# Kernel optimization log

Hardware: AMD Instinct MI355X
Metric: run time of the kernel (lower is better)

## Reference

```python
import jax, jax.numpy as jnp
import numpy as np

MODEL_DIM = 1024
NUM_HEADS = 16
HEAD_DIM = MODEL_DIM // NUM_HEADS
B, SQ, SK = 1, 4096, 4096


def setup_inputs() -> dict:
    key = jax.random.key(0)
    ks = jax.random.split(key, 10)
    s = 0.02  # realistic init scale for weights
    inp = {
        "x_query": jax.random.normal(ks[0], (B, SQ, MODEL_DIM), jnp.float32),
        "x_context": jax.random.normal(ks[1], (B, SK, MODEL_DIM), jnp.float32),
        # causal mask [B,1,Sq,Sk]; 0 -> masked
        "mask": jnp.tril(jnp.ones((SQ, SK), jnp.int32))[None, None, :, :],
        "wq": jax.random.normal(ks[2], (MODEL_DIM, MODEL_DIM), jnp.float32) * s,
        "bq": jnp.zeros((MODEL_DIM,), jnp.float32),
        "wk": jax.random.normal(ks[3], (MODEL_DIM, MODEL_DIM), jnp.float32) * s,
        "bk": jnp.zeros((MODEL_DIM,), jnp.float32),
        "wv": jax.random.normal(ks[4], (MODEL_DIM, MODEL_DIM), jnp.float32) * s,
        "bv": jnp.zeros((MODEL_DIM,), jnp.float32),
        "wo": jax.random.normal(ks[5], (MODEL_DIM, MODEL_DIM), jnp.float32) * s,
        "bo": jnp.zeros((MODEL_DIM,), jnp.float32),
    }
    return inp


def reference(x_query, x_context, mask, wq, bq, wk, bk, wv, bv, wo, bo):
    b = x_query.shape[0]
    # torch nn.Linear: y = x @ W.T + b
    q = x_query @ wq.T + bq
    k = x_context @ wk.T + bk
    v = x_context @ wv.T + bv
    # [B, S, D] -> [B, H, S, Hd]
    def split_heads(t):
        return t.reshape(b, -1, NUM_HEADS, HEAD_DIM).transpose(0, 2, 1, 3)
    q, k, v = split_heads(q), split_heads(k), split_heads(v)
    scale = 1.0 / jnp.sqrt(jnp.asarray(HEAD_DIM, q.dtype))
    scores = jnp.einsum('bhqd,bhkd->bhqk', q, k) * scale  # [B,H,Sq,Sk]
    scores = jnp.where(mask == 0, jnp.asarray(-1e9, scores.dtype), scores)
    attn = jax.nn.softmax(scores, axis=-1)
    # dropout: eval mode (identity)
    ctx = jnp.einsum('bhqk,bhkd->bhqd', attn, v)
    ctx = ctx.transpose(0, 2, 1, 3).reshape(b, -1, MODEL_DIM)
    return ctx @ wo.T + bo
```

## Files before the change

kernel.cpp:

```cpp
#include <hip/hip_runtime.h>

typedef __bf16 bf16x8 __attribute__((ext_vector_type(8)));
typedef float f32x4 __attribute__((ext_vector_type(4)));
typedef float f32x16 __attribute__((ext_vector_type(16)));
typedef unsigned int u32x2v __attribute__((ext_vector_type(2)));

#define GLD16(gp, lp) __builtin_amdgcn_global_load_lds( \
    (const __attribute__((address_space(1))) void*)(gp), \
    (__attribute__((address_space(3))) void*)(lp), 16, 0, 0)

__device__ __forceinline__ unsigned short f2bf(float f) {
  unsigned int u = __float_as_uint(f);
  u += 0x7FFFu + ((u >> 16) & 1u);
  return (unsigned short)(u >> 16);
}

__device__ __forceinline__ unsigned int cvtpk(float lo, float hi) {
  unsigned int r;
  asm("v_cvt_pk_bf16_f32 %0, %1, %2" : "=v"(r) : "v"(lo), "v"(hi));
  return r;
}

__device__ __forceinline__ float exp2f_(float x) {
#if __has_builtin(__builtin_amdgcn_exp2f)
  return __builtin_amdgcn_exp2f(x);
#else
  float r; asm("v_exp_f32 %0, %1" : "=v"(r) : "v"(x)); return r;
#endif
}

__device__ __forceinline__ u32x2v pswap(unsigned int a, unsigned int b) {
#if __has_builtin(__builtin_amdgcn_permlane32_swap)
  u32x2v r;
  auto q = __builtin_amdgcn_permlane32_swap(a, b, false, false);
  r[0] = q[0]; r[1] = q[1];
  return r;
#else
  unsigned int pa = (unsigned int)__shfl_xor((int)a, 32);
  unsigned int pb = (unsigned int)__shfl_xor((int)b, 32);
  int hi = (threadIdx.x >> 5) & 1;
  u32x2v r;
  r[0] = hi ? pb : a;
  r[1] = hi ? b : pa;
  return r;
#endif
}

__global__ __launch_bounds__(256) void cast6(
    const float* __restrict__ xq, const float* __restrict__ xc,
    const float* __restrict__ wq, const float* __restrict__ wk,
    const float* __restrict__ wv, const float* __restrict__ wo,
    unsigned short* __restrict__ d) {
  int i = (blockIdx.x * 256 + threadIdx.x) * 4;
  const float* s; int off;
  if      (i < (4 << 20))  { s = xq; off = 0; }
  else if (i < (8 << 20))  { s = xc; off = 4 << 20; }
  else if (i < (9 << 20))  { s = wq; off = 8 << 20; }
  else if (i < (10 << 20)) { s = wk; off = 9 << 20; }
  else if (i < (11 << 20)) { s = wv; off = 10 << 20; }
  else                     { s = wo; off = 11 << 20; }
  float4 v = *(const float4*)(s + (i - off));
  ushort4 o;
  o.x = f2bf(v.x); o.y = f2bf(v.y); o.z = f2bf(v.z); o.w = f2bf(v.w);
  *(ushort4*)(d + i) = o;
}

template<int OUTF32>
__device__ __forceinline__ void gemm_body(
    const unsigned short* __restrict__ A, const unsigned short* __restrict__ B,
    const float* __restrict__ bias, void* __restrict__ C,
    int N, int K, int bm, int bn, float scale,
    unsigned short* As, unsigned short* Bs) {
  const int t = threadIdx.x;
  const int lane = t & 63, wid = t >> 6;
  const int wm = wid >> 1, wn = wid & 1;
  const int l15 = lane & 15, l4 = lane >> 4, l7 = lane & 7;

  f32x4 acc[4][4];
#pragma unroll
  for (int i = 0; i < 4; ++i)
#pragma unroll
    for (int j = 0; j < 4; ++j) acc[i][j] = (f32x4){0.f, 0.f, 0.f, 0.f};

  const char* Ab = (const char*)A;
  const char* Bb = (const char*)B;
  const int ldb = K * 2;

  for (int kt = 0; kt < K; kt += 64) {
#pragma unroll
    for (int c = 0; c < 4; ++c) {
      int o = c * 4096 + wid * 1024 + lane * 16;
      int row = o >> 7;
      int ch = ((o >> 4) & 7) ^ (row & 7);
      const char* ga = Ab + (size_t)(bm * 128 + row) * ldb + kt * 2 + ch * 16;
      GLD16(ga, (char*)As + c * 4096 + wid * 1024);
      const char* gb = Bb + (size_t)(bn * 128 + row) * ldb + kt * 2 + ch * 16;
      GLD16(gb, (char*)Bs + c * 4096 + wid * 1024);
    }
    __syncthreads();
#pragma unroll
    for (int kk = 0; kk < 2; ++kk) {
      bf16x8 af[4], bfr[4];
#pragma unroll
      for (int mi = 0; mi < 4; ++mi) {
        int row = wm * 64 + mi * 16 + l15;
        int ch = (l4 + 4 * kk) ^ l7;
        af[mi] = *(const bf16x8*)((const char*)As + row * 128 + ch * 16);
      }
#pragma unroll
      for (int ni = 0; ni < 4; ++ni) {
        int row = wn * 64 + ni * 16 + l15;
        int ch = (l4 + 4 * kk) ^ l7;
        bfr[ni] = *(const bf16x8*)((const char*)Bs + row * 128 + ch * 16);
      }
#pragma unroll
      for (int mi = 0; mi < 4; ++mi)
#pragma unroll
        for (int ni = 0; ni < 4; ++ni)
          acc[mi][ni] = __builtin_amdgcn_mfma_f32_16x16x32_bf16(
              af[mi], bfr[ni], acc[mi][ni], 0, 0, 0);
    }
    __syncthreads();
  }

#pragma unroll
  for (int ni = 0; ni < 4; ++ni) {
    int col = bn * 128 + wn * 64 + ni * 16 + l15;
    float bv = bias[col];
#pragma unroll
    for (int mi = 0; mi < 4; ++mi) {
#pragma unroll
      for (int r = 0; r < 4; ++r) {
        int row = bm * 128 + wm * 64 + mi * 16 + l4 * 4 + r;
        float v = (acc[mi][ni][r] + bv) * scale;
        if (OUTF32) ((float*)C)[(size_t)row * N + col] = v;
        else ((unsigned short*)C)[(size_t)row * N + col] = f2bf(v);
      }
    }
  }
}

__global__ __launch_bounds__(256) void gemm_qkv(
    const unsigned short* __restrict__ xq, const unsigned short* __restrict__ xc,
    const unsigned short* __restrict__ wq, const unsigned short* __restrict__ wk,
    const unsigned short* __restrict__ wv,
    const float* __restrict__ bq, const float* __restrict__ bk,
    const float* __restrict__ bv,
    unsigned short* __restrict__ Qo, unsigned short* __restrict__ Ko,
    unsigned short* __restrict__ Vo) {
  __shared__ __align__(16) unsigned short As[128 * 64];
  __shared__ __align__(16) unsigned short Bs[128 * 64];
  const unsigned short* A; const unsigned short* B; const float* bias;
  unsigned short* C; float scale;
  if (blockIdx.z == 0)      { A = xq; B = wq; bias = bq; C = Qo; scale = 0.18033688011112042f; }
  else if (blockIdx.z == 1) { A = xc; B = wk; bias = bk; C = Ko; scale = 1.0f; }
  else                      { A = xc; B = wv; bias = bv; C = Vo; scale = 1.0f; }
  gemm_body<0>(A, B, bias, (void*)C, 1024, 1024, blockIdx.y, blockIdx.x, scale, As, Bs);
}

__global__ __launch_bounds__(256) void gemm_out(
    const unsigned short* __restrict__ A, const unsigned short* __restrict__ B,
    const float* __restrict__ bias, float* __restrict__ C) {
  __shared__ __align__(16) unsigned short As[128 * 64];
  __shared__ __align__(16) unsigned short Bs[128 * 64];
  gemm_body<1>(A, B, bias, (void*)C, 1024, 1024, blockIdx.y, blockIdx.x, 1.0f, As, Bs);
}

__global__ __launch_bounds__(512)
__attribute__((amdgpu_waves_per_eu(4, 4)))
void flash_attn(
    const unsigned short* __restrict__ Q, const unsigned short* __restrict__ K,
    const unsigned short* __restrict__ V, unsigned short* __restrict__ O) {
  __shared__ __align__(16) char smem[65536];

  const int wgid = blockIdx.x;
  int h, qb;
  if (wgid < 256) { h = wgid & 15; qb = wgid >> 4; }
  else            { int r = wgid - 256; h = r & 15; qb = 31 - (r >> 4); }

  const int t = threadIdx.x;
  const int lane = t & 63, w = t >> 6;
  const int hf = w >> 2;
  const int s = w & 3;
  const int tl = t & 255;
  const int l31 = lane & 31, hi = lane >> 5;
  const int q0w = qb * 128 + s * 32;
  const int qwmax = q0w + 31;
  const int nh = qb + 1;
  const int tbase = hf ? nh : 0;

  bf16x8 qf[4];
#pragma unroll
  for (int ks = 0; ks < 4; ++ks)
    qf[ks] = *(const bf16x8*)(Q + (size_t)(q0w + l31) * 1024 + h * 64 + ks * 16 + hi * 8);

  f32x16 po0, po1;
#pragma unroll
  for (int r = 0; r < 16; ++r) { po0[r] = 0.f; po1[r] = 0.f; }
  float m_i = -1e30f, l_i = 0.f;

  const int vd4 = (tl & 15) * 4;
  const int vkvr = (tl >> 4) * 4;
  uint2 va[4];

  auto stageK = [&](int tile, int buf) {
#pragma unroll
    for (int i = 0; i < 2; ++i) {
      int id = i * 256 + tl;
      int row = id >> 3;
      int ch = (id & 7) ^ (row & 7);
      GLD16((const char*)K + (size_t)(tile * 64 + row) * 2048 + h * 128 + ch * 16,
            smem + (hf * 2 + buf) * 8192 + id * 16);
    }
  };
  auto loadV = [&](int tile) {
#pragma unroll
    for (int i = 0; i < 4; ++i)
      va[i] = *(const uint2*)(V + (size_t)(tile * 64 + vkvr + i) * 1024 + h * 64 + vd4);
  };
  auto writeV = [&](int buf) {
    char* Vt = smem + 32768 + (hf * 2 + buf) * 8192;
#pragma unroll
    for (int j = 0; j < 4; ++j) {
      unsigned sel = (j & 1) ? 0x07060302u : 0x05040100u;
      unsigned s01 = (j < 2) ? __builtin_amdgcn_perm(va[1].x, va[0].x, sel)
                             : __builtin_amdgcn_perm(va[1].y, va[0].y, sel);
      unsigned s23 = (j < 2) ? __builtin_amdgcn_perm(va[3].x, va[2].x, sel)
                             : __builtin_amdgcn_perm(va[3].y, va[2].y, sel);
      int row = vd4 + j;
      int sw = (vkvr * 2) ^ (((row >> 2) & 7) << 4);
      *(uint2*)(Vt + row * 128 + sw) = make_uint2(s01, s23);
    }
  };

  stageK(tbase, 0);
  loadV(tbase);
  writeV(0);
  __syncthreads();

  for (int it = 0; it < nh; ++it) {
    const int c = it & 1;
    const bool pf = (it + 1) < nh;
    if (pf) { stageK(tbase + it + 1, c ^ 1); loadV(tbase + it + 1); }

    const int kv0 = (tbase + it) * 64;
    if (kv0 <= qwmax) {
      const char* Ks = smem + (hf * 2 + c) * 8192;
      const char* Vt = smem + 32768 + (hf * 2 + c) * 8192;
      f32x16 s0, s1;
#pragma unroll
      for (int r = 0; r < 16; ++r) { s0[r] = 0.f; s1[r] = 0.f; }
      __builtin_amdgcn_s_setprio(1);
#pragma unroll
      for (int ks = 0; ks < 4; ++ks) {
        int c0 = ((ks * 2 + hi) ^ (l31 & 7)) << 4;
        bf16x8 k0 = *(const bf16x8*)(Ks + l31 * 128 + c0);
        bf16x8 k1 = *(const bf16x8*)(Ks + (32 + l31) * 128 + c0);
        s0 = __builtin_amdgcn_mfma_f32_32x32x16_bf16(k0, qf[ks], s0, 0, 0, 0);
        s1 = __builtin_amdgcn_mfma_f32_32x32x16_bf16(k1, qf[ks], s1, 0, 0, 0);
      }
      __builtin_amdgcn_s_setprio(0);
      if (kv0 + 63 > q0w) {
        int q = q0w + l31;
#pragma unroll
        for (int r = 0; r < 16; ++r) {
          int kvi = kv0 + (r & 3) + 8 * (r >> 2) + 4 * hi;
          if (kvi > q) s0[r] = -1e30f;
          if (kvi + 32 > q) s1[r] = -1e30f;
        }
      }
      float mx[16];
#pragma unroll
      for (int i = 0; i < 8; ++i) {
        mx[i] = fmaxf(s0[2 * i], s0[2 * i + 1]);
        mx[8 + i] = fmaxf(s1[2 * i], s1[2 * i + 1]);
      }
#pragma unroll
      for (int i = 0; i < 8; ++i) mx[i] = fmaxf(mx[i], mx[8 + i]);
#pragma unroll
      for (int i = 0; i < 4; ++i) mx[i] = fmaxf(mx[i], mx[4 + i]);
      float mt = fmaxf(fmaxf(mx[0], mx[1]), fmaxf(mx[2], mx[3]));
      u32x2v mw = pswap(__float_as_uint(mt), __float_as_uint(mt));
      mt = fmaxf(__uint_as_float(mw[0]), __uint_as_float(mw[1]));
      if (!__all(mt - m_i <= 8.0f)) {
        float mn = fmaxf(m_i, mt);
        float corr = exp2f_(m_i - mn);
        m_i = mn;
        l_i *= corr;
#pragma unroll
        for (int r = 0; r < 16; ++r) { po0[r] *= corr; po1[r] *= corr; }
      }
#pragma unroll
      for (int r = 0; r < 16; ++r) s0[r] = exp2f_(s0[r] - m_i);
#pragma unroll
      for (int r = 0; r < 16; ++r) s1[r] = exp2f_(s1[r] - m_i);
      float sx[16];
#pragma unroll
      for (int i = 0; i < 8; ++i) {
        sx[i] = s0[2 * i] + s0[2 * i + 1];
        sx[8 + i] = s1[2 * i] + s1[2 * i + 1];
      }
#pragma unroll
      for (int i = 0; i < 8; ++i) sx[i] += sx[8 + i];
#pragma unroll
      for (int i = 0; i < 4; ++i) sx[i] += sx[4 + i];
      float ps = (sx[0] + sx[1]) + (sx[2] + sx[3]);
      u32x2v sw2 = pswap(__float_as_uint(ps), __float_as_uint(ps));
      l_i += __uint_as_float(sw2[0]) + __uint_as_float(sw2[1]);

#pragma unroll
      for (int kp = 0; kp < 4; ++kp) {
        const f32x16& sv = (kp < 2) ? s0 : s1;
        const int b = (kp & 1) * 8;
        unsigned c0v = cvtpk(sv[b + 0], sv[b + 1]);
        unsigned c1v = cvtpk(sv[b + 2], sv[b + 3]);
        unsigned c2v = cvtpk(sv[b + 4], sv[b + 5]);
        unsigned c3v = cvtpk(sv[b + 6], sv[b + 7]);
        u32x2v w02 = pswap(c0v, c2v);
        u32x2v w13 = pswap(c1v, c3v);
        union { unsigned u[4]; bf16x8 v; } pfr;
        pfr.u[0] = w02[0]; pfr.u[1] = w13[0]; pfr.u[2] = w02[1]; pfr.u[3] = w13[1];
        int cb = kp * 2 + hi;
        __builtin_amdgcn_s_setprio(1);
        {
          int row = l31;
          bf16x8 vf = *(const bf16x8*)(Vt + row * 128 + ((cb ^ ((row >> 2) & 7)) << 4));
          po0 = __builtin_amdgcn_mfma_f32_32x32x16_bf16(vf, pfr.v, po0, 0, 0, 0);
        }
        {
          int row = 32 + l31;
          bf16x8 vf = *(const bf16x8*)(Vt + row * 128 + ((cb ^ ((row >> 2) & 7)) << 4));
          po1 = __builtin_amdgcn_mfma_f32_32x32x16_bf16(vf, pfr.v, po1, 0, 0, 0);
        }
        __builtin_amdgcn_s_setprio(0);
      }
    }
    if (pf) writeV(c ^ 1);
    __syncthreads();
  }

  char* mrg = smem + 16384;
  if (hf) {
    char* mb = mrg + s * 9216 + lane * 144;
    *(f32x16*)(mb) = po0;
    *(f32x16*)(mb + 64) = po1;
    *(float*)(mb + 128) = m_i;
    *(float*)(mb + 132) = l_i;
  }
  __syncthreads();
  float rinv = 0.f;
  if (!hf) {
    char* mb = mrg + s * 9216 + lane * 144;
    float pm = *(float*)(mb + 128);
    float plv = *(float*)(mb + 132);
    float M = fmaxf(m_i, pm);
    float wA = exp2f_(m_i - M);
    float wB = exp2f_(pm - M);
    float lt = l_i * wA + plv * wB;
    rinv = 1.0f / lt;
    f32x16 qa = *(const f32x16*)(mb);
#pragma unroll
    for (int r = 0; r < 16; ++r) po0[r] = po0[r] * wA + qa[r] * wB;
    f32x16 qbv = *(const f32x16*)(mb + 64);
#pragma unroll
    for (int r = 0; r < 16; ++r) po1[r] = po1[r] * wA + qbv[r] * wB;

    int qlocal = s * 32 + l31;
#pragma unroll
    for (int g = 0; g < 4; ++g) {
#pragma unroll
      for (int db = 0; db < 2; ++db) {
        const f32x16& p = db ? po1 : po0;
        unsigned w0 = cvtpk(p[g * 4 + 0] * rinv, p[g * 4 + 1] * rinv);
        unsigned w1 = cvtpk(p[g * 4 + 2] * rinv, p[g * 4 + 3] * rinv);
        int d0 = db * 32 + 8 * g + 4 * hi;
        int byte = qlocal * 128 + ((d0 * 2) ^ ((qlocal & 7) << 4));
        *(uint2*)(smem + byte) = make_uint2(w0, w1);
      }
    }
  }
  __syncthreads();
  if (!hf) {
#pragma unroll
    for (int it = 0; it < 4; ++it) {
      int r = it * 32 + (t >> 3);
      int c = t & 7;
      uint4 val = *(const uint4*)(smem + r * 128 + ((c ^ (r & 7)) << 4));
      *(uint4*)((char*)O + (size_t)(qb * 128 + r) * 2048 + h * 128 + c * 16) = val;
    }
  }
}

extern "C" void kernel_launch(void* const* d_in, const int* in_sizes, int n_in,
                              void* d_out, int out_size, void* d_ws, size_t ws_size,
                              hipStream_t stream) {
  const float* xq = (const float*)d_in[0];
  const float* xc = (const float*)d_in[1];
  const float* wq = (const float*)d_in[3];
  const float* bq = (const float*)d_in[4];
  const float* wk = (const float*)d_in[5];
  const float* bk = (const float*)d_in[6];
  const float* wv = (const float*)d_in[7];
  const float* bv = (const float*)d_in[8];
  const float* wo = (const float*)d_in[9];
  const float* bo = (const float*)d_in[10];

  unsigned short* wsb = (unsigned short*)d_ws;
  unsigned short* xqb = wsb;
  unsigned short* xcb = wsb + (4 << 20);
  unsigned short* wqb = wsb + (8 << 20);
  unsigned short* wkb = wsb + (9 << 20);
  unsigned short* wvb = wsb + (10 << 20);
  unsigned short* wob = wsb + (11 << 20);
  unsigned short* Qb  = wsb + (12 << 20);
  unsigned short* Kb  = wsb + (16 << 20);
  unsigned short* Vb  = wsb + (20 << 20);
  unsigned short* Cb  = wsb + (24 << 20);

  cast6<<<12288, 256, 0, stream>>>(xq, xc, wq, wk, wv, wo, wsb);

  dim3 gq(1024 / 128, 4096 / 128, 3);
  gemm_qkv<<<gq, 256, 0, stream>>>(xqb, xcb, wqb, wkb, wvb, bq, bk, bv, Qb, Kb, Vb);

  flash_attn<<<512, 512, 0, stream>>>(Qb, Kb, Vb, Cb);

  dim3 go(1024 / 128, 4096 / 128);
  gemm_out<<<go, 256, 0, stream>>>(Cb, wob, bo, (float*)d_out);
}
```

Measured before the change: 160.7 us.

## Split long causal attention rows across two workgroups with atomic-flag merge

Changes the flash-attention work split. Instead of pairing a short and a long query block in one workgroup, short query blocks run alone and the long ones (qb >= 17) are split across two workgroups, which merge partial outputs through global scratch plus an atomic counter; the last one to arrive combines and stores. This aims to balance per-workgroup work and fill more CUs with 752 workgroups. The cost is an extra memset, fp32 partial writes and reads through global memory, and a scratch area that reuses the workspace where the bf16 casts of the inputs live (already consumed by that point).

```diff
diff --git a/kernel.cpp b/kernel.cpp
--- a/kernel.cpp
+++ b/kernel.cpp
@@ -166,17 +166,20 @@
   gemm_body<1>(A, B, bias, (void*)C, 1024, 1024, blockIdx.y, blockIdx.x, 1.0f, As, Bs);
 }
 
-__global__ __launch_bounds__(512)
-__attribute__((amdgpu_waves_per_eu(4, 4)))
+__global__ __launch_bounds__(512, 4)
 void flash_attn(
     const unsigned short* __restrict__ Q, const unsigned short* __restrict__ K,
-    const unsigned short* __restrict__ V, unsigned short* __restrict__ O) {
+    const unsigned short* __restrict__ V, unsigned short* __restrict__ O,
+    float* __restrict__ partO, float* __restrict__ mlBase,
+    int* __restrict__ flags) {
   __shared__ __align__(16) char smem[65536];
 
-  const int wgid = blockIdx.x;
-  int h, qb;
-  if (wgid < 256) { h = wgid & 15; qb = wgid >> 4; }
-  else            { int r = wgid - 256; h = r & 15; qb = 31 - (r >> 4); }
+  const int b = blockIdx.x;
+  const int h = b & 15;
+  const int e = 46 - (b >> 4);
+  int qb, role, nsplit;
+  if (e < 17) { qb = e; role = 0; nsplit = 1; }
+  else        { qb = 17 + ((e - 17) >> 1); role = (e - 17) & 1; nsplit = 2; }
 
   const int t = threadIdx.x;
   const int lane = t & 63, w = t >> 6;
@@ -186,8 +189,12 @@
   const int l31 = lane & 31, hi = lane >> 5;
   const int q0w = qb * 128 + s * 32;
   const int qwmax = q0w + 31;
-  const int nh = qb + 1;
-  const int tbase = hf ? nh : 0;
+
+  const int t0 = (nsplit == 2) ? role * (qb + 1) : 0;
+  const int n  = (nsplit == 2) ? (qb + 1) : 2 * (qb + 1);
+  const int nA = (n + 1) >> 1;
+  const int my_n = hf ? (n - nA) : nA;
+  const int my_t0 = t0 + (hf ? nA : 0);
 
   bf16x8 qf[4];
 #pragma unroll
@@ -233,109 +240,109 @@
     }
   };
 
-  stageK(tbase, 0);
-  loadV(tbase);
-  writeV(0);
+  if (my_n > 0) { stageK(my_t0, 0); loadV(my_t0); writeV(0); }
   __syncthreads();
 
-  for (int it = 0; it < nh; ++it) {
+  for (int it = 0; it < nA; ++it) {
     const int c = it & 1;
-    const bool pf = (it + 1) < nh;
-    if (pf) { stageK(tbase + it + 1, c ^ 1); loadV(tbase + it + 1); }
-
-    const int kv0 = (tbase + it) * 64;
-    if (kv0 <= qwmax) {
-      const char* Ks = smem + (hf * 2 + c) * 8192;
-      const char* Vt = smem + 32768 + (hf * 2 + c) * 8192;
-      f32x16 s0, s1;
-#pragma unroll
-      for (int r = 0; r < 16; ++r) { s0[r] = 0.f; s1[r] = 0.f; }
-      __builtin_amdgcn_s_setprio(1);
-#pragma unroll
-      for (int ks = 0; ks < 4; ++ks) {
-        int c0 = ((ks * 2 + hi) ^ (l31 & 7)) << 4;
-        bf16x8 k0 = *(const bf16x8*)(Ks + l31 * 128 + c0);
-        bf16x8 k1 = *(const bf16x8*)(Ks + (32 + l31) * 128 + c0);
-        s0 = __builtin_amdgcn_mfma_f32_32x32x16_bf16(k0, qf[ks], s0, 0, 0, 0);
-        s1 = __builtin_amdgcn_mfma_f32_32x32x16_bf16(k1, qf[ks], s1, 0, 0, 0);
-      }
-      __builtin_amdgcn_s_setprio(0);
-      if (kv0 + 63 > q0w) {
-        int q = q0w + l31;
-#pragma unroll
-        for (int r = 0; r < 16; ++r) {
-          int kvi = kv0 + (r & 3) + 8 * (r >> 2) + 4 * hi;
-          if (kvi > q) s0[r] = -1e30f;
-          if (kvi + 32 > q) s1[r] = -1e30f;
-        }
-      }
-      float mx[16];
-#pragma unroll
-      for (int i = 0; i < 8; ++i) {
-        mx[i] = fmaxf(s0[2 * i], s0[2 * i + 1]);
-        mx[8 + i] = fmaxf(s1[2 * i], s1[2 * i + 1]);
-      }
-#pragma unroll
-      for (int i = 0; i < 8; ++i) mx[i] = fmaxf(mx[i], mx[8 + i]);
-#pragma unroll
-      for (int i = 0; i < 4; ++i) mx[i] = fmaxf(mx[i], mx[4 + i]);
-      float mt = fmaxf(fmaxf(mx[0], mx[1]), fmaxf(mx[2], mx[3]));
-      u32x2v mw = pswap(__float_as_uint(mt), __float_as_uint(mt));
-      mt = fmaxf(__uint_as_float(mw[0]), __uint_as_float(mw[1]));
-      if (!__all(mt - m_i <= 8.0f)) {
-        float mn = fmaxf(m_i, mt);
-        float corr = exp2f_(m_i - mn);
-        m_i = mn;
-        l_i *= corr;
-#pragma unroll
-        for (int r = 0; r < 16; ++r) { po0[r] *= corr; po1[r] *= corr; }
-      }
-#pragma unroll
-      for (int r = 0; r < 16; ++r) s0[r] = exp2f_(s0[r] - m_i);
-#pragma unroll
-      for (int r = 0; r < 16; ++r) s1[r] = exp2f_(s1[r] - m_i);
-      float sx[16];
-#pragma unroll
-      for (int i = 0; i < 8; ++i) {
-        sx[i] = s0[2 * i] + s0[2 * i + 1];
-        sx[8 + i] = s1[2 * i] + s1[2 * i + 1];
-      }
-#pragma unroll
-      for (int i = 0; i < 8; ++i) sx[i] += sx[8 + i];
-#pragma unroll
-      for (int i = 0; i < 4; ++i) sx[i] += sx[4 + i];
-      float ps = (sx[0] + sx[1]) + (sx[2] + sx[3]);
-      u32x2v sw2 = pswap(__float_as_uint(ps), __float_as_uint(ps));
-      l_i += __uint_as_float(sw2[0]) + __uint_as_float(sw2[1]);
-
-#pragma unroll
-      for (int kp = 0; kp < 4; ++kp) {
-        const f32x16& sv = (kp < 2) ? s0 : s1;
-        const int b = (kp & 1) * 8;
-        unsigned c0v = cvtpk(sv[b + 0], sv[b + 1]);
-        unsigned c1v = cvtpk(sv[b + 2], sv[b + 3]);
-        unsigned c2v = cvtpk(sv[b + 4], sv[b + 5]);
-        unsigned c3v = cvtpk(sv[b + 6], sv[b + 7]);
-        u32x2v w02 = pswap(c0v, c2v);
-        u32x2v w13 = pswap(c1v, c3v);
-        union { unsigned u[4]; bf16x8 v; } pfr;
-        pfr.u[0] = w02[0]; pfr.u[1] = w13[0]; pfr.u[2] = w02[1]; pfr.u[3] = w13[1];
-        int cb = kp * 2 + hi;
+    const bool pfv = (it + 1) < my_n;
+    if (pfv) { stageK(my_t0 + it + 1, c ^ 1); loadV(my_t0 + it + 1); }
+
+    if (it < my_n) {
+      const int kv0 = (my_t0 + it) * 64;
+      if (kv0 <= qwmax) {
+        const char* Ks = smem + (hf * 2 + c) * 8192;
+        const char* Vt = smem + 32768 + (hf * 2 + c) * 8192;
+        f32x16 s0, s1;
+#pragma unroll
+        for (int r = 0; r < 16; ++r) { s0[r] = 0.f; s1[r] = 0.f; }
         __builtin_amdgcn_s_setprio(1);
-        {
-          int row = l31;
-          bf16x8 vf = *(const bf16x8*)(Vt + row * 128 + ((cb ^ ((row >> 2) & 7)) << 4));
-          po0 = __builtin_amdgcn_mfma_f32_32x32x16_bf16(vf, pfr.v, po0, 0, 0, 0);
-        }
-        {
-          int row = 32 + l31;
-          bf16x8 vf = *(const bf16x8*)(Vt + row * 128 + ((cb ^ ((row >> 2) & 7)) << 4));
-          po1 = __builtin_amdgcn_mfma_f32_32x32x16_bf16(vf, pfr.v, po1, 0, 0, 0);
+#pragma unroll
+        for (int ks = 0; ks < 4; ++ks) {
+          int c0 = ((ks * 2 + hi) ^ (l31 & 7)) << 4;
+          bf16x8 k0 = *(const bf16x8*)(Ks + l31 * 128 + c0);
+          bf16x8 k1 = *(const bf16x8*)(Ks + (32 + l31) * 128 + c0);
+          s0 = __builtin_amdgcn_mfma_f32_32x32x16_bf16(k0, qf[ks], s0, 0, 0, 0);
+          s1 = __builtin_amdgcn_mfma_f32_32x32x16_bf16(k1, qf[ks], s1, 0, 0, 0);
         }
         __builtin_amdgcn_s_setprio(0);
-      }
-    }
-    if (pf) writeV(c ^ 1);
+        if (kv0 + 63 > q0w) {
+          int q = q0w + l31;
+#pragma unroll
+          for (int r = 0; r < 16; ++r) {
+            int kvi = kv0 + (r & 3) + 8 * (r >> 2) + 4 * hi;
+            if (kvi > q) s0[r] = -1e30f;
+            if (kvi + 32 > q) s1[r] = -1e30f;
+          }
+        }
+        float mx[16];
+#pragma unroll
+        for (int i = 0; i < 8; ++i) {
+          mx[i] = fmaxf(s0[2 * i], s0[2 * i + 1]);
+          mx[8 + i] = fmaxf(s1[2 * i], s1[2 * i + 1]);
+        }
+#pragma unroll
+        for (int i = 0; i < 8; ++i) mx[i] = fmaxf(mx[i], mx[8 + i]);
+#pragma unroll
+        for (int i = 0; i < 4; ++i) mx[i] = fmaxf(mx[i], mx[4 + i]);
+        float mt = fmaxf(fmaxf(mx[0], mx[1]), fmaxf(mx[2], mx[3]));
+        u32x2v mw = pswap(__float_as_uint(mt), __float_as_uint(mt));
+        mt = fmaxf(__uint_as_float(mw[0]), __uint_as_float(mw[1]));
+        if (!__all(mt - m_i <= 8.0f)) {
+          float mn = fmaxf(m_i, mt);
+          float corr = exp2f_(m_i - mn);
+          m_i = mn;
+          l_i *= corr;
+#pragma unroll
+          for (int r = 0; r < 16; ++r) { po0[r] *= corr; po1[r] *= corr; }
+        }
+#pragma unroll
+        for (int r = 0; r < 16; ++r) s0[r] = exp2f_(s0[r] - m_i);
+#pragma unroll
+        for (int r = 0; r < 16; ++r) s1[r] = exp2f_(s1[r] - m_i);
+        float sx[16];
+#pragma unroll
+        for (int i = 0; i < 8; ++i) {
+          sx[i] = s0[2 * i] + s0[2 * i + 1];
+          sx[8 + i] = s1[2 * i] + s1[2 * i + 1];
+        }
+#pragma unroll
+        for (int i = 0; i < 8; ++i) sx[i] += sx[8 + i];
+#pragma unroll
+        for (int i = 0; i < 4; ++i) sx[i] += sx[4 + i];
+        float ps = (sx[0] + sx[1]) + (sx[2] + sx[3]);
+        u32x2v sw2 = pswap(__float_as_uint(ps), __float_as_uint(ps));
+        l_i += __uint_as_float(sw2[0]) + __uint_as_float(sw2[1]);
+
+#pragma unroll
+        for (int kp = 0; kp < 4; ++kp) {
+          const f32x16& sv = (kp < 2) ? s0 : s1;
+          const int bb = (kp & 1) * 8;
+          unsigned c0v = cvtpk(sv[bb + 0], sv[bb + 1]);
+          unsigned c1v = cvtpk(sv[bb + 2], sv[bb + 3]);
+          unsigned c2v = cvtpk(sv[bb + 4], sv[bb + 5]);
+          unsigned c3v = cvtpk(sv[bb + 6], sv[bb + 7]);
+          u32x2v w02 = pswap(c0v, c2v);
+          u32x2v w13 = pswap(c1v, c3v);
+          union { unsigned u[4]; bf16x8 v; } pfr;
+          pfr.u[0] = w02[0]; pfr.u[1] = w13[0]; pfr.u[2] = w02[1]; pfr.u[3] = w13[1];
+          int cb = kp * 2 + hi;
+          __builtin_amdgcn_s_setprio(1);
+          {
+            int row = l31;
+            bf16x8 vf = *(const bf16x8*)(Vt + row * 128 + ((cb ^ ((row >> 2) & 7)) << 4));
+            po0 = __builtin_amdgcn_mfma_f32_32x32x16_bf16(vf, pfr.v, po0, 0, 0, 0);
+          }
+          {
+            int row = 32 + l31;
+            bf16x8 vf = *(const bf16x8*)(Vt + row * 128 + ((cb ^ ((row >> 2) & 7)) << 4));
+            po1 = __builtin_amdgcn_mfma_f32_32x32x16_bf16(vf, pfr.v, po1, 0, 0, 0);
+          }
+          __builtin_amdgcn_s_setprio(0);
+        }
+      }
+    }
+    if (pfv) writeV(c ^ 1);
     __syncthreads();
   }
 
@@ -348,7 +355,6 @@
     *(float*)(mb + 132) = l_i;
   }
   __syncthreads();
-  float rinv = 0.f;
   if (!hf) {
     char* mb = mrg + s * 9216 + lane * 144;
     float pm = *(float*)(mb + 128);
@@ -356,37 +362,91 @@
     float M = fmaxf(m_i, pm);
     float wA = exp2f_(m_i - M);
     float wB = exp2f_(pm - M);
-    float lt = l_i * wA + plv * wB;
-    rinv = 1.0f / lt;
+    l_i = l_i * wA + plv * wB;
+    m_i = M;
     f32x16 qa = *(const f32x16*)(mb);
 #pragma unroll
     for (int r = 0; r < 16; ++r) po0[r] = po0[r] * wA + qa[r] * wB;
     f32x16 qbv = *(const f32x16*)(mb + 64);
 #pragma unroll
     for (int r = 0; r < 16; ++r) po1[r] = po1[r] * wA + qbv[r] * wB;
-
-    int qlocal = s * 32 + l31;
-#pragma unroll
-    for (int g = 0; g < 4; ++g) {
-#pragma unroll
-      for (int db = 0; db < 2; ++db) {
-        const f32x16& p = db ? po1 : po0;
-        unsigned w0 = cvtpk(p[g * 4 + 0] * rinv, p[g * 4 + 1] * rinv);
-        unsigned w1 = cvtpk(p[g * 4 + 2] * rinv, p[g * 4 + 3] * rinv);
-        int d0 = db * 32 + 8 * g + 4 * hi;
-        int byte = qlocal * 128 + ((d0 * 2) ^ ((qlocal & 7) << 4));
-        *(uint2*)(smem + byte) = make_uint2(w0, w1);
-      }
-    }
-  }
-  __syncthreads();
-  if (!hf) {
-#pragma unroll
-    for (int it = 0; it < 4; ++it) {
-      int r = it * 32 + (t >> 3);
-      int c = t & 7;
-      uint4 val = *(const uint4*)(smem + r * 128 + ((c ^ (r & 7)) << 4));
-      *(uint4*)((char*)O + (size_t)(qb * 128 + r) * 2048 + h * 128 + c * 16) = val;
+  }
+
+  bool doStore;
+  float rinv = 1.0f;
+  if (nsplit == 1) {
+    doStore = true;
+    rinv = 1.0f / l_i;
+  } else {
+    const int pairIdx = h * 15 + (qb - 17);
+    if (!hf) {
+      float* baseO = partO + (size_t)pairIdx * 16384 + role * 8192;
+      int laneSlot = s * 64 + hi * 32 + l31;
+      *(f32x16*)(baseO + laneSlot * 32) = po0;
+      *(f32x16*)(baseO + laneSlot * 32 + 16) = po1;
+      if (!hi) {
+        float* mlp = mlBase + (size_t)pairIdx * 512 + role * 256 + (s * 32 + l31) * 2;
+        mlp[0] = m_i;
+        mlp[1] = l_i;
+      }
+    }
+    __syncthreads();
+    if (t == 0) {
+      __threadfence();
+      int old = atomicAdd(flags + pairIdx, 1);
+      *(volatile int*)(smem + 16384) = old;
+    }
+    __syncthreads();
+    int old = *(volatile int*)(smem + 16384);
+    doStore = (old == 1);
+    if (doStore) {
+      __threadfence();
+      if (!hf) {
+        const float* baseP = partO + (size_t)pairIdx * 16384;
+        int laneSlot = s * 64 + hi * 32 + l31;
+        f32x16 A0 = *(const f32x16*)(baseP + laneSlot * 32);
+        f32x16 A1 = *(const f32x16*)(baseP + laneSlot * 32 + 16);
+        f32x16 B0 = *(const f32x16*)(baseP + 8192 + laneSlot * 32);
+        f32x16 B1 = *(const f32x16*)(baseP + 8192 + laneSlot * 32 + 16);
+        const float* mlp = mlBase + (size_t)pairIdx * 512 + (s * 32 + l31) * 2;
+        float m0 = mlp[0], l0v = mlp[1];
+        float m1 = mlp[256], l1v = mlp[257];
+        float M = fmaxf(m0, m1);
+        float w0 = exp2f_(m0 - M), w1 = exp2f_(m1 - M);
+        rinv = 1.0f / (l0v * w0 + l1v * w1);
+#pragma unroll
+        for (int r = 0; r < 16; ++r) po0[r] = A0[r] * w0 + B0[r] * w1;
+#pragma unroll
+        for (int r = 0; r < 16; ++r) po1[r] = A1[r] * w0 + B1[r] * w1;
+      }
+    }
+  }
+
+  if (doStore) {
+    if (!hf) {
+      int qlocal = s * 32 + l31;
+#pragma unroll
+      for (int g = 0; g < 4; ++g) {
+#pragma unroll
+        for (int db = 0; db < 2; ++db) {
+          const f32x16& p = db ? po1 : po0;
+          unsigned w0 = cvtpk(p[g * 4 + 0] * rinv, p[g * 4 + 1] * rinv);
+          unsigned w1 = cvtpk(p[g * 4 + 2] * rinv, p[g * 4 + 3] * rinv);
+          int d0 = db * 32 + 8 * g + 4 * hi;
+          int byte = qlocal * 128 + ((d0 * 2) ^ ((qlocal & 7) << 4));
+          *(uint2*)(smem + byte) = make_uint2(w0, w1);
+        }
+      }
+    }
+    __syncthreads();
+    if (!hf) {
+#pragma unroll
+      for (int it = 0; it < 4; ++it) {
+        int r = it * 32 + (t >> 3);
+        int c = t & 7;
+        uint4 val = *(const uint4*)(smem + r * 128 + ((c ^ (r & 7)) << 4));
+        *(uint4*)((char*)O + (size_t)(qb * 128 + r) * 2048 + h * 128 + c * 16) = val;
+      }
     }
   }
 }
@@ -417,12 +477,18 @@
   unsigned short* Vb  = wsb + (20 << 20);
   unsigned short* Cb  = wsb + (24 << 20);
 
+  float* partO  = (float*)d_ws;
+  float* mlBase = (float*)((char*)d_ws + (16u << 20));
+  int*   flags  = (int*)((char*)d_ws + (17u << 20));
+
   cast6<<<12288, 256, 0, stream>>>(xq, xc, wq, wk, wv, wo, wsb);
 
   dim3 gq(1024 / 128, 4096 / 128, 3);
   gemm_qkv<<<gq, 256, 0, stream>>>(xqb, xcb, wqb, wkb, wvb, bq, bk, bv, Qb, Kb, Vb);
 
-  flash_attn<<<512, 512, 0, stream>>>(Qb, Kb, Vb, Cb);
+  hipMemsetAsync(flags, 0, 240 * sizeof(int), stream);
+
+  flash_attn<<<752, 512, 0, stream>>>(Qb, Kb, Vb, Cb, partO, mlBase, flags);
 
   dim3 go(1024 / 128, 4096 / 128);
   gemm_out<<<go, 256, 0, stream>>>(Cb, wob, bo, (float*)d_out);
```

Measured after the change: 246.0 us. 1.53x slower.
